# Optimization experiments

Measured on AMD Instinct MI355X. Metric: run time of the kernel, lower is better.

Reference implementation:

```python
import jax, jax.numpy as jnp
import numpy as np

ALPHA = 0.0001
BETA = 0.75
K_CONST = 1.0
N_WIN = 5


def setup_inputs() -> dict:
    key = jax.random.key(0)
    x = jax.random.normal(key, (64, 56, 56, 192), dtype=jnp.float32)
    return {"x": x}


def reference(x):
    # Faithful reproduction of the (buggy) keras LRN:
    #   head = max(c - half_n, 0)
    #   tail = min(c + half_n, C)
    #   window = x_sqr[..., head : c + tail + 1]  (end clipped to C by slicing)
    C = x.shape[-1]
    half_n = N_WIN // 2
    x_sqr = x * x
    # Exclusive-prefix cumsum along channels: cs[..., j] = sum of x_sqr[..., :j]
    cs = jnp.concatenate(
        [jnp.zeros(x.shape[:-1] + (1,), x.dtype), jnp.cumsum(x_sqr, axis=-1)],
        axis=-1,
    )  # [B,H,W,C+1]
    c = np.arange(C)
    head = np.maximum(c - half_n, 0)
    tail = np.minimum(c + half_n, C)
    end = np.minimum(c + tail + 1, C)  # python slicing clips the stop index
    # windowed sum-of-squares per output channel via prefix-sum difference
    scale = cs[..., end] - cs[..., head]  # [B,H,W,C]
    scale = (scale * (ALPHA / N_WIN) + K_CONST) ** BETA
    return x / scale
```

## Files before the change

### kernel.cpp

```cpp
#include <hip/hip_runtime.h>


constexpr int   C     = 192;
constexpr int   LPP   = 16;
constexpr int   PPW   = 4;
constexpr int   WPB   = 4;
constexpr int   PPB   = PPW * WPB;
constexpr int   BLOCK = 256;
constexpr float AON   = 0.0001f / 5.0f;

__device__ __forceinline__ float bperm(int byteaddr, float v) {
  return __int_as_float(__builtin_amdgcn_ds_bpermute(byteaddr, __float_as_int(v)));
}

__global__ __launch_bounds__(BLOCK, 6) void lrn_kernel(
    const float* __restrict__ x, float* __restrict__ out, int npix) {
  const int tid  = threadIdx.x;
  const int lane = tid & 63;
  const int w    = tid >> 6;
  const int sub  = lane & 15;
  const int pl   = lane >> 4;

  long long pix = (long long)blockIdx.x * PPB + w * PPW + pl;
  if (pix > npix - 1) pix = npix - 1;

  const float4* __restrict__ xb = (const float4*)(x + (size_t)pix * C);
  float4* __restrict__ ob       = (float4*)(out + (size_t)pix * C);

  const float4 u0 = xb[sub];
  const float4 u1 = xb[16 + sub];
  const float4 u2 = xb[32 + sub];

  float xs[3][4] = {{u0.x, u0.y, u0.z, u0.w},
                    {u1.x, u1.y, u1.z, u1.w},
                    {u2.x, u2.y, u2.z, u2.w}};

  float q[3];
#pragma unroll
  for (int s = 0; s < 3; ++s)
    q[s] = fmaf(xs[s][0], xs[s][0],
           fmaf(xs[s][1], xs[s][1],
           fmaf(xs[s][2], xs[s][2], xs[s][3] * xs[s][3])));

  float i0 = q[0], i1 = q[1], i2 = q[2];
#pragma unroll
  for (int off = 1; off < LPP; off <<= 1) {
    const float t0 = __shfl_up(i0, off, LPP);
    const float t1 = __shfl_up(i1, off, LPP);
    const float t2 = __shfl_up(i2, off, LPP);
    if (sub >= off) { i0 += t0; i1 += t1; i2 += t2; }
  }
  const float T0 = __shfl(i0, LPP - 1, LPP);
  const float T1 = __shfl(i1, LPP - 1, LPP);
  const float T2 = __shfl(i2, LPP - 1, LPP);
  const float total = T0 + T1 + T2;
  const float E[3] = { i0 - q[0], T0 + i1 - q[1], T0 + T1 + i2 - q[2] };

  float p[3][4];
#pragma unroll
  for (int s = 0; s < 3; ++s) {
    float run = E[s];
#pragma unroll
    for (int k = 0; k < 4; ++k) { p[s][k] = run; run = fmaf(xs[s][k], xs[s][k], run); }
  }

  float hb0[3], hb1[3];
#pragma unroll
  for (int s = 0; s < 3; ++s) {
    hb0[s] = __shfl_up(p[s][2], 1, LPP);
    hb1[s] = __shfl_up(p[s][3], 1, LPP);
  }
  const float B02 = __shfl(p[0][2], LPP - 1, LPP);
  const float B03 = __shfl(p[0][3], LPP - 1, LPP);
  const float B12 = __shfl(p[1][2], LPP - 1, LPP);
  const float B13 = __shfl(p[1][3], LPP - 1, LPP);
  if (sub == 0) {
    hb0[0] = 0.0f; hb1[0] = 0.0f;
    hb0[1] = B02;  hb1[1] = B03;
    hb0[2] = B12;  hb1[2] = B13;
  }

  const int gb = lane & 48;
  const int a0 = (gb | ((2 * sub)     & 15)) << 2;
  const int a1 = (gb | ((2 * sub + 1) & 15)) << 2;
  const int a2 = (gb | ((2 * sub + 2) & 15)) << 2;

  float ge0[4], ge1[4];
  {
    const float r00 = bperm(a0, p[0][3]), r01 = bperm(a0, p[1][3]);
    const float r10 = bperm(a1, p[0][1]), r11 = bperm(a1, p[1][1]);
    const float r20 = bperm(a1, p[0][3]), r21 = bperm(a1, p[1][3]);
    const float r30 = bperm(a2, p[0][1]), r31 = bperm(a2, p[1][1]);
    ge0[0] = (sub < 8) ? r00 : r01;
    ge0[1] = (sub < 8) ? r10 : r11;
    ge0[2] = (sub < 8) ? r20 : r21;
    ge0[3] = (sub < 7) ? r30 : r31;
    ge1[0] = bperm(a0, p[2][3]);
    ge1[1] = bperm(a1, p[2][1]);
    ge1[2] = bperm(a1, p[2][3]);
    ge1[3] = bperm(a2, p[2][1]);
  }

#pragma unroll
  for (int s = 0; s < 3; ++s) {
    float r[4];
#pragma unroll
    for (int k = 0; k < 4; ++k) {
      const float csh = (k >= 2) ? p[s][k - 2] : (k == 0 ? hb0[s] : hb1[s]);
      float cse;
      if (s == 0)      cse = ge0[k];
      else if (s == 1) cse = (4 * sub + k >= 31) ? total : ge1[k];
      else             cse = total;
      const float eps = (cse - csh) * AON;
      const float inv = fmaf(eps, fmaf(eps, fmaf(eps, -0.6015625f, 0.65625f), -0.75f), 1.0f);
      r[k] = xs[s][k] * inv;
    }
    ob[16 * s + sub] = make_float4(r[0], r[1], r[2], r[3]);
  }
}

extern "C" void kernel_launch(void* const* d_in, const int* in_sizes, int n_in,
                              void* d_out, int out_size, void* d_ws, size_t ws_size,
                              hipStream_t stream) {
  const float* x   = (const float*)d_in[0];
  float*       out = (float*)d_out;
  const int npix = in_sizes[0] / C;
  const int grid = (npix + PPB - 1) / PPB;
  lrn_kernel<<<grid, BLOCK, 0, stream>>>(x, out, npix);
}
```

Before: 259.9 us.

## Use persistent grid-stride loop with register prefetch and nontemporal stores

```diff
diff --git a/kernel.cpp b/kernel.cpp
--- a/kernel.cpp
+++ b/kernel.cpp
@@ -5,32 +5,25 @@
 constexpr int   LPP   = 16;
 constexpr int   PPW   = 4;
 constexpr int   WPB   = 4;
-constexpr int   PPB   = PPW * WPB;
 constexpr int   BLOCK = 256;
+constexpr int   GRID  = 1792;
 constexpr float AON   = 0.0001f / 5.0f;
+
+typedef float f32x4 __attribute__((ext_vector_type(4)));
 
 __device__ __forceinline__ float bperm(int byteaddr, float v) {
   return __int_as_float(__builtin_amdgcn_ds_bpermute(byteaddr, __float_as_int(v)));
 }
 
-__global__ __launch_bounds__(BLOCK, 6) void lrn_kernel(
-    const float* __restrict__ x, float* __restrict__ out, int npix) {
-  const int tid  = threadIdx.x;
-  const int lane = tid & 63;
-  const int w    = tid >> 6;
-  const int sub  = lane & 15;
-  const int pl   = lane >> 4;
+__device__ __forceinline__ void nt_store4(float a, float b, float c, float d,
+                                          float4* __restrict__ p) {
+  f32x4 t = {a, b, c, d};
+  __builtin_nontemporal_store(t, (f32x4*)p);
+}
 
-  long long pix = (long long)blockIdx.x * PPB + w * PPW + pl;
-  if (pix > npix - 1) pix = npix - 1;
-
-  const float4* __restrict__ xb = (const float4*)(x + (size_t)pix * C);
-  float4* __restrict__ ob       = (float4*)(out + (size_t)pix * C);
-
-  const float4 u0 = xb[sub];
-  const float4 u1 = xb[16 + sub];
-  const float4 u2 = xb[32 + sub];
-
+__device__ __forceinline__ void lrn_body(const float4 u0, const float4 u1, const float4 u2,
+                                         float4* __restrict__ ob, int sub,
+                                         int a0, int a1, int a2) {
   float xs[3][4] = {{u0.x, u0.y, u0.z, u0.w},
                     {u1.x, u1.y, u1.z, u1.w},
                     {u2.x, u2.y, u2.z, u2.w}};
@@ -80,11 +73,6 @@
     hb0[2] = B12;  hb1[2] = B13;
   }
 
-  const int gb = lane & 48;
-  const int a0 = (gb | ((2 * sub)     & 15)) << 2;
-  const int a1 = (gb | ((2 * sub + 1) & 15)) << 2;
-  const int a2 = (gb | ((2 * sub + 2) & 15)) << 2;
-
   float ge0[4], ge1[4];
   {
     const float r00 = bperm(a0, p[0][3]), r01 = bperm(a0, p[1][3]);
@@ -115,7 +103,50 @@
       const float inv = fmaf(eps, fmaf(eps, fmaf(eps, -0.6015625f, 0.65625f), -0.75f), 1.0f);
       r[k] = xs[s][k] * inv;
     }
-    ob[16 * s + sub] = make_float4(r[0], r[1], r[2], r[3]);
+    nt_store4(r[0], r[1], r[2], r[3], &ob[16 * s + sub]);
+  }
+}
+
+__global__ __launch_bounds__(BLOCK, 4) void lrn_kernel(
+    const float* __restrict__ x, float* __restrict__ out, int npix) {
+  const int tid  = threadIdx.x;
+  const int lane = tid & 63;
+  const int w    = tid >> 6;
+  const int sub  = lane & 15;
+  const int pl   = lane >> 4;
+
+  const int slot   = blockIdx.x * WPB + w;
+  const int nslots = gridDim.x * WPB;
+  const int ngrp   = (npix + PPW - 1) / PPW;
+  int nit = (ngrp - slot + nslots - 1) / nslots;
+  if (nit <= 0) return;
+
+  const int gb = lane & 48;
+  const int a0 = (gb | ((2 * sub)     & 15)) << 2;
+  const int a1 = (gb | ((2 * sub + 1) & 15)) << 2;
+  const int a2 = (gb | ((2 * sub + 2) & 15)) << 2;
+
+  const float4* __restrict__ xb = (const float4*)x;
+  const int nclamp = npix - 1;
+
+  int grp = slot;
+  int pix = grp * PPW + pl; if (pix > nclamp) pix = nclamp;
+  int fb  = pix * (C / 4) + sub;
+  float4 A0 = xb[fb], A1 = xb[fb + 16], A2 = xb[fb + 32];
+
+  for (int t = 0; t < nit; ++t) {
+    const int curfb = fb;
+    const int gn = grp + nslots;
+    float4 B0, B1, B2;
+    if (t + 1 < nit) {
+      int pixn = gn * PPW + pl; if (pixn > nclamp) pixn = nclamp;
+      fb = pixn * (C / 4) + sub;
+      B0 = xb[fb]; B1 = xb[fb + 16]; B2 = xb[fb + 32];
+    }
+    float4* ob = (float4*)out + (curfb - sub);
+    lrn_body(A0, A1, A2, ob, sub, a0, a1, a2);
+    grp = gn;
+    A0 = B0; A1 = B1; A2 = B2;
   }
 }
 
@@ -125,6 +156,8 @@
   const float* x   = (const float*)d_in[0];
   float*       out = (float*)d_out;
   const int npix = in_sizes[0] / C;
-  const int grid = (npix + PPB - 1) / PPB;
+  const int ngrp = (npix + PPW - 1) / PPW;
+  int grid = (ngrp + WPB - 1) / WPB;
+  if (grid > GRID) grid = GRID;
   lrn_kernel<<<grid, BLOCK, 0, stream>>>(x, out, npix);
 }
```

Measured after the change: 265.6 us. 1.02x slower.
